# Kernel optimization log

Measured on AMD Instinct MI355X. Metric: run time of the kernel, lower is better.

Reference implementation:

```python
import jax, jax.numpy as jnp
import numpy as np


def setup_inputs() -> dict:
    key = jax.random.key(0)
    k1, k2, k3, k4 = jax.random.split(key, 4)
    N, C, H, W = 4, 256, 64, 64
    Co, kh, kw, dg = 256, 3, 3, 1
    x = jax.random.normal(k1, (N, C, H, W), dtype=jnp.float32)
    offset = jax.random.normal(k2, (N, 2 * dg * kh * kw, H, W), dtype=jnp.float32)
    mask = jax.random.uniform(k3, (N, dg * kh * kw, H, W), dtype=jnp.float32)
    weight = jax.random.normal(k4, (Co, C, kh, kw), dtype=jnp.float32) * 0.02
    bias = jnp.zeros((Co,), dtype=jnp.float32)
    return {"x": x, "offset": offset, "mask": mask, "weight": weight, "bias": bias,
            "stride": 1, "padding": 1, "dilation": 1, "deformable_groups": 1}


def _dcn_v2(x, offset, mask, weight, bias, stride, padding, dilation, dg):
    N, C, H, W = x.shape
    Co, Ci, kh, kw = weight.shape
    K = kh * kw
    Ho, Wo = offset.shape[2], offset.shape[3]
    Cg = C // dg

    off = offset.reshape(N, dg, K, 2, Ho, Wo)
    dy, dx = off[:, :, :, 0], off[:, :, :, 1]          # [N,dg,K,Ho,Wo]
    m = mask.reshape(N, dg, K, Ho, Wo)

    ki = (jnp.arange(K) // kw).astype(jnp.float32)      # kernel row index
    kj = (jnp.arange(K) % kw).astype(jnp.float32)       # kernel col index
    base_y = (jnp.arange(Ho, dtype=jnp.float32) * stride - padding)
    base_x = (jnp.arange(Wo, dtype=jnp.float32) * stride - padding)
    # sampling coordinates [N,dg,K,Ho,Wo]
    py = dy + base_y[None, None, None, :, None] + (ki * dilation)[None, None, :, None, None]
    px = dx + base_x[None, None, None, None, :] + (kj * dilation)[None, None, :, None, None]

    y0 = jnp.floor(py)
    x0 = jnp.floor(px)
    wy1 = py - y0
    wx1 = px - x0
    wy0 = 1.0 - wy1
    wx0 = 1.0 - wx1
    y0i = y0.astype(jnp.int32)
    x0i = x0.astype(jnp.int32)

    xr = x.reshape(N, dg, Cg, H * W)

    def gather(yi, xi):
        valid = ((yi >= 0) & (yi < H) & (xi >= 0) & (xi < W)).astype(x.dtype)
        idx = jnp.clip(yi, 0, H - 1) * W + jnp.clip(xi, 0, W - 1)   # [N,dg,K,Ho,Wo]
        flat = idx.reshape(N, dg, 1, K * Ho * Wo)
        g = jnp.take_along_axis(xr, flat, axis=-1).reshape(N, dg, Cg, K, Ho, Wo)
        return g * valid[:, :, None]

    sampled = (gather(y0i, x0i) * (wy0 * wx0)[:, :, None]
               + gather(y0i, x0i + 1) * (wy0 * wx1)[:, :, None]
               + gather(y0i + 1, x0i) * (wy1 * wx0)[:, :, None]
               + gather(y0i + 1, x0i + 1) * (wy1 * wx1)[:, :, None])
    sampled = sampled * m[:, :, None]                     # modulation
    sampled = sampled.reshape(N, C, K, Ho, Wo)

    out = jnp.einsum('nckhw,ock->nohw', sampled, weight.reshape(Co, C, K))
    return out + bias[None, :, None, None]


def reference(x, offset, mask, weight, bias, stride, padding, dilation, deformable_groups):
    return _dcn_v2(x, offset, mask, weight, bias, stride, padding, dilation, deformable_groups)
```

## Files before the change

### kernel.cpp

```cpp
#include <hip/hip_runtime.h>


typedef _Float16 f16x8 __attribute__((ext_vector_type(8)));
typedef _Float16 f16x4 __attribute__((ext_vector_type(4)));
typedef float f32x4 __attribute__((ext_vector_type(4)));

#define C_IN 256
#define CO   256
#define KK   9
#define HWSZ 4096
#define LDB  72
#define BUFB (64 * LDB)

struct __align__(16) SP { ushort4 idx; f16x4 w; };

static __device__ __forceinline__ f16x8 splat8(_Float16 v) {
    f16x8 r = {v, v, v, v, v, v, v, v};
    return r;
}

__global__ void transpose_x_kernel(const float* __restrict__ x,
                                   _Float16* __restrict__ xt) {
    __shared__ float tile[64][65];
    const int n  = blockIdx.z;
    const int p0 = blockIdx.x * 64;
    const int c0 = blockIdx.y * 64;
    const int tx = threadIdx.x & 63;
    const int ty = threadIdx.x >> 6;
    for (int i = 0; i < 16; ++i) {
        int c = ty * 16 + i;
        tile[c][tx] = x[((size_t)(n * C_IN + c0 + c) << 12) + p0 + tx];
    }
    __syncthreads();
    for (int i = 0; i < 16; ++i) {
        int p = ty * 16 + i;
        xt[((size_t)((n << 12) + p0 + p) << 8) + c0 + tx] = (_Float16)tile[tx][p];
    }
}

__global__ void transpose_w_kernel(const float* __restrict__ w,
                                   _Float16* __restrict__ wt2) {
    const int o = blockIdx.x;
    const int c = threadIdx.x;
    const int f = o >> 4, r = o & 15, cc = c >> 5, kq = c & 31;
    for (int kk = 0; kk < KK; ++kk) {
        int q = cc * 9 + kk;
        wt2[((f * 72 + q) * 16 + r) * 32 + kq] =
            (_Float16)w[(o * C_IN + c) * KK + kk];
    }
}

template <int NHALF>
__launch_bounds__(256, 2)
__global__ void dcn_main_kernel(const float* __restrict__ offset,
                                const float* __restrict__ mask,
                                const float* __restrict__ bias,
                                const _Float16* __restrict__ xt,
                                const _Float16* __restrict__ wt2,
                                float* __restrict__ out0,
                                float* __restrict__ out1) {
    constexpr int NS = 36 / NHALF;
    __shared__ SP sP[576];
    __shared__ _Float16 sB[2][BUFB];

    const int tid = threadIdx.x;
    const int cpx = (256 * NHALF) >> 3;
    const int lin = blockIdx.x;
    const int id  = (lin & 7) * cpx + (lin >> 3);
    const int half = (NHALF == 2) ? (id >> 8) : 0;
    const int pt   = id & 255;
    const int p0   = pt * 64;
    const int n    = p0 >> 12;
    const int phw0 = p0 & 4095;
    const int cc0  = half * 4;

    for (int t = tid; t < 576; t += 256) {
        int pl = t / 9;
        int k  = t - pl * 9;
        int phw = phw0 + pl;
        int h = phw >> 6, w = phw & 63;
        float dy = offset[(size_t)(n * 18 + 2 * k)     * HWSZ + phw];
        float dx = offset[(size_t)(n * 18 + 2 * k + 1) * HWSZ + phw];
        float mv = mask  [(size_t)(n * 9 + k)          * HWSZ + phw];
        float py = dy + (float)(h - 1 + k / 3);
        float px = dx + (float)(w - 1 + k % 3);
        float y0f = floorf(py), x0f = floorf(px);
        int y0 = (int)y0f, x0 = (int)x0f;
        float wy1 = py - y0f, wx1 = px - x0f;
        float wy0 = 1.f - wy1, wx0 = 1.f - wx1;
        int y1 = y0 + 1, x1 = x0 + 1;
        float vy0 = (y0 >= 0 && y0 < 64) ? 1.f : 0.f;
        float vy1 = (y1 >= 0 && y1 < 64) ? 1.f : 0.f;
        float vx0 = (x0 >= 0 && x0 < 64) ? 1.f : 0.f;
        float vx1 = (x1 >= 0 && x1 < 64) ? 1.f : 0.f;
        int cy0 = min(max(y0, 0), 63), cy1 = min(max(y1, 0), 63);
        int cx0 = min(max(x0, 0), 63), cx1 = min(max(x1, 0), 63);
        SP e;
        e.idx = make_ushort4((unsigned short)(cy0 * 64 + cx0),
                             (unsigned short)(cy0 * 64 + cx1),
                             (unsigned short)(cy1 * 64 + cx0),
                             (unsigned short)(cy1 * 64 + cx1));
        f16x4 wv;
        wv.x = (_Float16)(wy0 * wx0 * mv * vy0 * vx0);
        wv.y = (_Float16)(wy0 * wx1 * mv * vy0 * vx1);
        wv.z = (_Float16)(wy1 * wx0 * mv * vy1 * vx0);
        wv.w = (_Float16)(wy1 * wx1 * mv * vy1 * vx1);
        e.w = wv;
        sP[t] = e;
    }
    __syncthreads();

    const int lane = tid & 63;
    const int wid  = tid >> 6;
    const int l15  = lane & 15;
    const int lhi  = lane >> 4;

    const int pixl  = tid >> 2;
    const int oct   = tid & 3;
    const int pixl9 = pixl * 9;

    const char* xb  = (const char*)(xt + ((size_t)n << 12) * C_IN);
    const char* wtb = (const char*)wt2;

    const int vBe = l15 * LDB + lhi * 8;
    const int vWe = pixl * LDB + oct * 8;

    unsigned voffA[4];
    for (int fm = 0; fm < 4; ++fm) {
        int fglob = wid * 4 + fm;
        voffA[fm] = (unsigned)((fglob * 72 + cc0 * 9) * 1024 + l15 * 64 + lhi * 16);
    }
    unsigned aOffB = 0;
    unsigned chB_E = cc0 * 64 + oct * 16;
    unsigned chB_O = cc0 * 64 + oct * 16;
    int kiE = 0, kiO = 1;

    f16x8 ga[8];
    f16x8 aa[8];
    f16x4 gw[2];
    f32x4 acc[4][4];
    for (int i = 0; i < 4; ++i)
        for (int j = 0; j < 4; ++j)
            acc[i][j] = (f32x4){0.f, 0.f, 0.f, 0.f};

#define ISSUE_GA()                                                            \
    {                                                                         \
        SP e0 = sP[pixl9 + kiE];                                              \
        SP e1 = sP[pixl9 + kiO];                                              \
        gw[0] = e0.w;                                                         \
        gw[1] = e1.w;                                                         \
        ga[0] = *(const f16x8*)(xb + (((unsigned)e0.idx.x << 9) + chB_E));    \
        ga[1] = *(const f16x8*)(xb + (((unsigned)e0.idx.y << 9) + chB_E));    \
        ga[2] = *(const f16x8*)(xb + (((unsigned)e0.idx.z << 9) + chB_E));    \
        ga[3] = *(const f16x8*)(xb + (((unsigned)e0.idx.w << 9) + chB_E));    \
        ga[4] = *(const f16x8*)(xb + (((unsigned)e1.idx.x << 9) + chB_O));    \
        ga[5] = *(const f16x8*)(xb + (((unsigned)e1.idx.y << 9) + chB_O));    \
        ga[6] = *(const f16x8*)(xb + (((unsigned)e1.idx.z << 9) + chB_O));    \
        ga[7] = *(const f16x8*)(xb + (((unsigned)e1.idx.w << 9) + chB_O));    \
        kiE += 2; if (kiE >= 9) { kiE -= 9; chB_E += 64; }                    \
        kiO += 2; if (kiO >= 9) { kiO -= 9; chB_O += 64; }                    \
    }

#define ISSUE_A()                                                             \
    {                                                                         \
        for (int fm_ = 0; fm_ < 4; ++fm_) {                                   \
            unsigned vo_ = voffA[fm_] + aOffB;                                \
            aa[fm_ * 2 + 0] = *(const f16x8*)(wtb + vo_);                     \
            aa[fm_ * 2 + 1] = *(const f16x8*)(wtb + vo_ + 1024);              \
        }                                                                     \
        aOffB += 2048;                                                        \
    }

#define COMBINE(BUFOFF)                                                       \
    {                                                                         \
        _Float16* bw_ = &sB[0][0] + (BUFOFF) + vWe;                           \
        f16x8 r0_ = ga[0] * splat8(gw[0].x) + ga[1] * splat8(gw[0].y)         \
                  + ga[2] * splat8(gw[0].z) + ga[3] * splat8(gw[0].w);        \
        f16x8 r1_ = ga[4] * splat8(gw[1].x) + ga[5] * splat8(gw[1].y)         \
                  + ga[6] * splat8(gw[1].z) + ga[7] * splat8(gw[1].w);        \
        *(f16x8*)(bw_)      = r0_;                                            \
        *(f16x8*)(bw_ + 32) = r1_;                                            \
    }

#define MFMA_STEP(BUFOFF)                                                     \
    {                                                                         \
        const _Float16* br_ = &sB[0][0] + (BUFOFF) + vBe;                     \
        for (int fn_ = 0; fn_ < 4; ++fn_) {                                   \
            f16x8 bE_ = *(const f16x8*)(br_ + fn_ * 16 * LDB);                \
            f16x8 bO_ = *(const f16x8*)(br_ + fn_ * 16 * LDB + 32);           \
            for (int fm_ = 0; fm_ < 4; ++fm_) {                               \
                acc[fm_][fn_] = __builtin_amdgcn_mfma_f32_16x16x32_f16(       \
                    aa[fm_ * 2 + 0], bE_, acc[fm_][fn_], 0, 0, 0);            \
                acc[fm_][fn_] = __builtin_amdgcn_mfma_f32_16x16x32_f16(       \
                    aa[fm_ * 2 + 1], bO_, acc[fm_][fn_], 0, 0, 0);            \
            }                                                                 \
        }                                                                     \
    }

#define BAR()                                                                 \
    {                                                                         \
        asm volatile("s_waitcnt lgkmcnt(0)" ::: "memory");                    \
        __builtin_amdgcn_s_barrier();                                         \
        asm volatile("" ::: "memory");                                        \
    }

    ISSUE_GA()
    COMBINE(0)
    BAR()

#pragma unroll 2
    for (int s = 0; s < NS; ++s) {
        ISSUE_A()
        if (s + 1 < NS) ISSUE_GA()
        MFMA_STEP((s & 1) * BUFB)
        if (s + 1 < NS) {
            COMBINE(((s + 1) & 1) * BUFB)
            BAR()
        }
    }

    float* po = (NHALF == 2 && half == 1) ? out1 : out0;
    for (int fm = 0; fm < 4; ++fm) {
        for (int fn = 0; fn < 4; ++fn) {
            int pix = phw0 + fn * 16 + l15;
            for (int r = 0; r < 4; ++r) {
                int o = wid * 64 + fm * 16 + lhi * 4 + r;
                float v = acc[fm][fn][r];
                if constexpr (NHALF == 1) v += bias[o];
                po[((size_t)(n * CO + o) << 12) + pix] = v;
            }
        }
    }
#undef ISSUE_GA
#undef ISSUE_A
#undef COMBINE
#undef MFMA_STEP
#undef BAR
}

__global__ void reduce_kernel(float* __restrict__ out,
                              const float* __restrict__ part,
                              const float* __restrict__ bias, int n4) {
    int i = blockIdx.x * blockDim.x + threadIdx.x;
    const int stride = gridDim.x * blockDim.x;
    for (; i < n4; i += stride) {
        f32x4 a = ((const f32x4*)out)[i];
        f32x4 b = ((const f32x4*)part)[i];
        float bv = bias[(i >> 10) & 255];
        a.x += b.x + bv; a.y += b.y + bv; a.z += b.z + bv; a.w += b.w + bv;
        ((f32x4*)out)[i] = a;
    }
}

extern "C" void kernel_launch(void* const* d_in, const int* in_sizes, int n_in,
                              void* d_out, int out_size, void* d_ws, size_t ws_size,
                              hipStream_t stream) {
    const float* x      = (const float*)d_in[0];
    const float* offset = (const float*)d_in[1];
    const float* mask   = (const float*)d_in[2];
    const float* weight = (const float*)d_in[3];
    const float* bias   = (const float*)d_in[4];
    float* out = (float*)d_out;

    _Float16* xt  = (_Float16*)d_ws;
    _Float16* wt2 = (_Float16*)((char*)d_ws + 8388608);
    float*  part1 = (float*)((char*)d_ws + 9568256);
    const bool split = ws_size >= (size_t)9568256 + (size_t)4 * CO * HWSZ * 4;

    transpose_x_kernel<<<dim3(64, 4, 4), 256, 0, stream>>>(x, xt);
    transpose_w_kernel<<<CO, C_IN, 0, stream>>>(weight, wt2);
    if (split) {
        dcn_main_kernel<2><<<dim3(512), 256, 0, stream>>>(offset, mask, bias,
                                                          xt, wt2, out, part1);
        reduce_kernel<<<dim3(2048), 256, 0, stream>>>(out, part1, bias,
                                                      (4 * CO * HWSZ) / 4);
    } else {
        dcn_main_kernel<1><<<dim3(256), 256, 0, stream>>>(offset, mask, bias,
                                                          xt, wt2, out, out);
    }
}
```

Before: 59.32 us.

## Deepen gather and weight prefetch to two stages with full unroll

Register prefetching gets deeper. The x gathers are now issued two steps ahead and the weight fragments one step ahead, using double-buffered register slots. The loop is fully unrolled so that tap and channel offsets become compile-time constants, and the shared sampling table now stores byte offsets that are already shifted, which removes per-iteration index arithmetic. A sched_barrier keeps the load issue ahead of the MFMAs. The cost is a doubling of the register arrays, which may cause spills or lower occupancy under launch_bounds(256,2), and larger code from the full unroll.

```diff
diff --git a/kernel.cpp b/kernel.cpp
--- a/kernel.cpp
+++ b/kernel.cpp
@@ -12,7 +12,7 @@
 #define LDB  72
 #define BUFB (64 * LDB)
 
-struct __align__(16) SP { ushort4 idx; f16x4 w; };
+struct __align__(16) SP2 { uint4 off; f16x4 w; };
 
 static __device__ __forceinline__ f16x8 splat8(_Float16 v) {
     f16x8 r = {v, v, v, v, v, v, v, v};
@@ -60,7 +60,7 @@
                                 float* __restrict__ out0,
                                 float* __restrict__ out1) {
     constexpr int NS = 36 / NHALF;
-    __shared__ SP sP[576];
+    __shared__ SP2 sP[576];
     __shared__ _Float16 sB[2][BUFB];
 
     const int tid = threadIdx.x;
@@ -95,11 +95,11 @@
         float vx1 = (x1 >= 0 && x1 < 64) ? 1.f : 0.f;
         int cy0 = min(max(y0, 0), 63), cy1 = min(max(y1, 0), 63);
         int cx0 = min(max(x0, 0), 63), cx1 = min(max(x1, 0), 63);
-        SP e;
-        e.idx = make_ushort4((unsigned short)(cy0 * 64 + cx0),
-                             (unsigned short)(cy0 * 64 + cx1),
-                             (unsigned short)(cy1 * 64 + cx0),
-                             (unsigned short)(cy1 * 64 + cx1));
+        SP2 e;
+        e.off = make_uint4((unsigned)(cy0 * 64 + cx0) << 9,
+                           (unsigned)(cy0 * 64 + cx1) << 9,
+                           (unsigned)(cy1 * 64 + cx0) << 9,
+                           (unsigned)(cy1 * 64 + cx1) << 9);
         f16x4 wv;
         wv.x = (_Float16)(wy0 * wx0 * mv * vy0 * vx0);
         wv.y = (_Float16)(wy0 * wx1 * mv * vy0 * vx1);
@@ -124,75 +124,75 @@
 
     const int vBe = l15 * LDB + lhi * 8;
     const int vWe = pixl * LDB + oct * 8;
+    const unsigned chBase = (unsigned)(cc0 * 64 + oct * 16);
 
     unsigned voffA[4];
     for (int fm = 0; fm < 4; ++fm) {
         int fglob = wid * 4 + fm;
         voffA[fm] = (unsigned)((fglob * 72 + cc0 * 9) * 1024 + l15 * 64 + lhi * 16);
     }
-    unsigned aOffB = 0;
-    unsigned chB_E = cc0 * 64 + oct * 16;
-    unsigned chB_O = cc0 * 64 + oct * 16;
-    int kiE = 0, kiO = 1;
-
-    f16x8 ga[8];
-    f16x8 aa[8];
-    f16x4 gw[2];
+
+    f16x8 ga[2][8];
+    f16x8 aa[2][8];
+    f16x4 gw[2][2];
     f32x4 acc[4][4];
     for (int i = 0; i < 4; ++i)
         for (int j = 0; j < 4; ++j)
             acc[i][j] = (f32x4){0.f, 0.f, 0.f, 0.f};
 
-#define ISSUE_GA()                                                            \
-    {                                                                         \
-        SP e0 = sP[pixl9 + kiE];                                              \
-        SP e1 = sP[pixl9 + kiO];                                              \
-        gw[0] = e0.w;                                                         \
-        gw[1] = e1.w;                                                         \
-        ga[0] = *(const f16x8*)(xb + (((unsigned)e0.idx.x << 9) + chB_E));    \
-        ga[1] = *(const f16x8*)(xb + (((unsigned)e0.idx.y << 9) + chB_E));    \
-        ga[2] = *(const f16x8*)(xb + (((unsigned)e0.idx.z << 9) + chB_E));    \
-        ga[3] = *(const f16x8*)(xb + (((unsigned)e0.idx.w << 9) + chB_E));    \
-        ga[4] = *(const f16x8*)(xb + (((unsigned)e1.idx.x << 9) + chB_O));    \
-        ga[5] = *(const f16x8*)(xb + (((unsigned)e1.idx.y << 9) + chB_O));    \
-        ga[6] = *(const f16x8*)(xb + (((unsigned)e1.idx.z << 9) + chB_O));    \
-        ga[7] = *(const f16x8*)(xb + (((unsigned)e1.idx.w << 9) + chB_O));    \
-        kiE += 2; if (kiE >= 9) { kiE -= 9; chB_E += 64; }                    \
-        kiO += 2; if (kiO >= 9) { kiO -= 9; chB_O += 64; }                    \
-    }
-
-#define ISSUE_A()                                                             \
+#define ISSUE_GA(T, SLOT)                                                     \
+    {                                                                         \
+        const SP2 e0 = sP[pixl9 + (2 * (T)) % 9];                             \
+        const SP2 e1 = sP[pixl9 + (2 * (T) + 1) % 9];                         \
+        gw[SLOT][0] = e0.w;                                                   \
+        gw[SLOT][1] = e1.w;                                                   \
+        const unsigned cE = chBase + (unsigned)(((2 * (T)) / 9) * 64);        \
+        const unsigned cO = chBase + (unsigned)(((2 * (T) + 1) / 9) * 64);    \
+        ga[SLOT][0] = *(const f16x8*)(xb + (e0.off.x + cE));                  \
+        ga[SLOT][1] = *(const f16x8*)(xb + (e0.off.y + cE));                  \
+        ga[SLOT][2] = *(const f16x8*)(xb + (e0.off.z + cE));                  \
+        ga[SLOT][3] = *(const f16x8*)(xb + (e0.off.w + cE));                  \
+        ga[SLOT][4] = *(const f16x8*)(xb + (e1.off.x + cO));                  \
+        ga[SLOT][5] = *(const f16x8*)(xb + (e1.off.y + cO));                  \
+        ga[SLOT][6] = *(const f16x8*)(xb + (e1.off.z + cO));                  \
+        ga[SLOT][7] = *(const f16x8*)(xb + (e1.off.w + cO));                  \
+    }
+
+#define ISSUE_A(T, SLOT)                                                      \
     {                                                                         \
         for (int fm_ = 0; fm_ < 4; ++fm_) {                                   \
-            unsigned vo_ = voffA[fm_] + aOffB;                                \
-            aa[fm_ * 2 + 0] = *(const f16x8*)(wtb + vo_);                     \
-            aa[fm_ * 2 + 1] = *(const f16x8*)(wtb + vo_ + 1024);              \
+            unsigned vo_ = voffA[fm_] + (unsigned)((T) * 2048);               \
+            aa[SLOT][fm_ * 2 + 0] = *(const f16x8*)(wtb + vo_);               \
+            aa[SLOT][fm_ * 2 + 1] = *(const f16x8*)(wtb + vo_ + 1024);        \
         }                                                                     \
-        aOffB += 2048;                                                        \
-    }
-
-#define COMBINE(BUFOFF)                                                       \
-    {                                                                         \
-        _Float16* bw_ = &sB[0][0] + (BUFOFF) + vWe;                           \
-        f16x8 r0_ = ga[0] * splat8(gw[0].x) + ga[1] * splat8(gw[0].y)         \
-                  + ga[2] * splat8(gw[0].z) + ga[3] * splat8(gw[0].w);        \
-        f16x8 r1_ = ga[4] * splat8(gw[1].x) + ga[5] * splat8(gw[1].y)         \
-                  + ga[6] * splat8(gw[1].z) + ga[7] * splat8(gw[1].w);        \
+    }
+
+#define COMBINE(SLOT, BUF)                                                    \
+    {                                                                         \
+        _Float16* bw_ = &sB[0][0] + (BUF) * BUFB + vWe;                       \
+        f16x8 r0_ = ga[SLOT][0] * splat8(gw[SLOT][0].x)                       \
+                  + ga[SLOT][1] * splat8(gw[SLOT][0].y)                       \
+                  + ga[SLOT][2] * splat8(gw[SLOT][0].z)                       \
+                  + ga[SLOT][3] * splat8(gw[SLOT][0].w);                      \
+        f16x8 r1_ = ga[SLOT][4] * splat8(gw[SLOT][1].x)                       \
+                  + ga[SLOT][5] * splat8(gw[SLOT][1].y)                       \
+                  + ga[SLOT][6] * splat8(gw[SLOT][1].z)                       \
+                  + ga[SLOT][7] * splat8(gw[SLOT][1].w);                      \
         *(f16x8*)(bw_)      = r0_;                                            \
         *(f16x8*)(bw_ + 32) = r1_;                                            \
     }
 
-#define MFMA_STEP(BUFOFF)                                                     \
-    {                                                                         \
-        const _Float16* br_ = &sB[0][0] + (BUFOFF) + vBe;                     \
+#define MFMA_STEP(SLOT, BUF)                                                  \
+    {                                                                         \
+        const _Float16* br_ = &sB[0][0] + (BUF) * BUFB + vBe;                 \
         for (int fn_ = 0; fn_ < 4; ++fn_) {                                   \
             f16x8 bE_ = *(const f16x8*)(br_ + fn_ * 16 * LDB);                \
             f16x8 bO_ = *(const f16x8*)(br_ + fn_ * 16 * LDB + 32);           \
             for (int fm_ = 0; fm_ < 4; ++fm_) {                               \
                 acc[fm_][fn_] = __builtin_amdgcn_mfma_f32_16x16x32_f16(       \
-                    aa[fm_ * 2 + 0], bE_, acc[fm_][fn_], 0, 0, 0);            \
+                    aa[SLOT][fm_ * 2 + 0], bE_, acc[fm_][fn_], 0, 0, 0);      \
                 acc[fm_][fn_] = __builtin_amdgcn_mfma_f32_16x16x32_f16(       \
-                    aa[fm_ * 2 + 1], bO_, acc[fm_][fn_], 0, 0, 0);            \
+                    aa[SLOT][fm_ * 2 + 1], bO_, acc[fm_][fn_], 0, 0, 0);      \
             }                                                                 \
         }                                                                     \
     }
@@ -204,17 +204,20 @@
         asm volatile("" ::: "memory");                                        \
     }
 
-    ISSUE_GA()
-    COMBINE(0)
+    ISSUE_GA(0, 0)
+    ISSUE_GA(1, 1)
+    ISSUE_A(0, 0)
+    COMBINE(0, 0)
     BAR()
 
-#pragma unroll 2
+#pragma unroll
     for (int s = 0; s < NS; ++s) {
-        ISSUE_A()
-        if (s + 1 < NS) ISSUE_GA()
-        MFMA_STEP((s & 1) * BUFB)
+        if (s + 1 < NS) ISSUE_A(s + 1, (s + 1) & 1)
+        if (s + 2 < NS) ISSUE_GA(s + 2, s & 1)
+        __builtin_amdgcn_sched_barrier(0);
+        MFMA_STEP(s & 1, s & 1)
         if (s + 1 < NS) {
-            COMBINE(((s + 1) & 1) * BUFB)
+            COMBINE((s + 1) & 1, (s + 1) & 1)
             BAR()
         }
     }
```

After: 55.34 us. 6.7% less time.
